# Kernel optimization log

Hardware: AMD Instinct MI355X
Metric: run time of the kernel (lower is better)

Reference implementation:

```python
import jax, jax.numpy as jnp
import numpy as np

EPS = 1e-8  # torch nn.CosineSimilarity default eps


def setup_inputs() -> dict:
    key = jax.random.key(0)
    k1, k2, k3 = jax.random.split(key, 3)
    N, K, Q, CH, H, W, D = 32, 5, 15, 3, 84, 84, 1600
    supp_x = jax.random.normal(k1, (N, K, CH, H, W), dtype=jnp.float32)
    query_x = jax.random.normal(k2, (N, Q, CH, H, W), dtype=jnp.float32)
    W_enc = jax.random.normal(k3, (CH * H * W, D), dtype=jnp.float32) * 0.02
    return {"supp_x": supp_x, "query_x": query_x, "W_enc": W_enc}


def reference(supp_x, query_x, W_enc):
    N, K = supp_x.shape[0], supp_x.shape[1]
    Q = query_x.shape[1]
    # encoder: flatten image -> linear projection (stands in for backbone)
    s_feat = supp_x.reshape(N * K, -1) @ W_enc          # (N*K, D)
    x_proto = s_feat.reshape(N, K, -1).mean(axis=1)     # (N, D) class prototypes
    x_q = query_x.reshape(N * Q, -1) @ W_enc            # (N*Q, D)
    # cosine similarity: L2-normalize with eps clamp, then single matmul
    qn = x_q / jnp.maximum(jnp.linalg.norm(x_q, axis=1, keepdims=True), EPS)
    pn = x_proto / jnp.maximum(jnp.linalg.norm(x_proto, axis=1, keepdims=True), EPS)
    sim = qn @ pn.T                                     # (N*Q, N)
    return jax.nn.log_softmax(sim, axis=1)
```

## Files before the change

kernel.cpp:

```cpp
#include <hip/hip_runtime.h>
#include <cstdint>
#include <cstddef>

namespace {

constexpr int NCLS   = 32;
constexpr int KSHOT  = 5;
constexpr int FDIM   = 21168;
constexpr int KPAD   = 21248;
constexpr int DDIM   = 1600;
constexpr int NROW   = 512;
constexpr int NQROW  = 480;
constexpr int NKT    = 332;
constexpr int MAXS   = 10;

using short8 = __attribute__((ext_vector_type(8))) short;
using f32x4  = __attribute__((ext_vector_type(4))) float;

__device__ __forceinline__ unsigned f2bf(float x) {
    union { float f; unsigned u; } v; v.f = x;
    unsigned r = v.u + 0x7fffu + ((v.u >> 16) & 1u);
    return r >> 16;
}

__global__ void prep_A(const float* __restrict__ supp,
                       const float* __restrict__ query,
                       unsigned short* __restrict__ A) {
    const int r = blockIdx.y;
    const int u = blockIdx.x * blockDim.x + threadIdx.x;
    if (u >= KPAD / 4) return;
    const int c = u * 4;
    float4 v = make_float4(0.f, 0.f, 0.f, 0.f);
    if (c < FDIM) {
        if (r < NCLS) {
            const float* s = supp + (size_t)r * KSHOT * FDIM + c;
            float4 a0 = *(const float4*)(s);
            float4 a1 = *(const float4*)(s + FDIM);
            float4 a2 = *(const float4*)(s + 2 * FDIM);
            float4 a3 = *(const float4*)(s + 3 * FDIM);
            float4 a4 = *(const float4*)(s + 4 * FDIM);
            v.x = (a0.x + a1.x + a2.x + a3.x + a4.x) * 0.2f;
            v.y = (a0.y + a1.y + a2.y + a3.y + a4.y) * 0.2f;
            v.z = (a0.z + a1.z + a2.z + a3.z + a4.z) * 0.2f;
            v.w = (a0.w + a1.w + a2.w + a3.w + a4.w) * 0.2f;
        } else {
            v = *(const float4*)(query + (size_t)(r - NCLS) * FDIM + c);
        }
    }
    ushort4 o;
    o.x = (unsigned short)f2bf(v.x); o.y = (unsigned short)f2bf(v.y);
    o.z = (unsigned short)f2bf(v.z); o.w = (unsigned short)f2bf(v.w);
    *(ushort4*)(A + (size_t)r * KPAD + c) = o;
}

__global__ __launch_bounds__(512, 4) void gemm10(
        const unsigned short* __restrict__ A,
        const float* __restrict__ W,
        float* __restrict__ Cpart, int S) {
    __shared__ unsigned short Al[2][256 * 64];
    __shared__ unsigned short Bl[2][64 * 64];

    const int nwg = gridDim.x, orig = blockIdx.x;
    const int xcd = orig & 7, q8 = nwg >> 3, r8 = nwg & 7;
    const int wgid = (xcd < r8 ? xcd * (q8 + 1) : r8 * (q8 + 1) + (xcd - r8) * q8)
                   + (orig >> 3);

    const int s   = wgid / 50;
    const int rem = wgid % 50;
    const int mt  = rem / 25;
    const int nt  = rem % 25;
    const int m0  = mt * 256;
    const int n0  = nt * 64;
    const int t0  = (NKT * s) / S;
    const int t1  = (NKT * (s + 1)) / S;
    const int tmax = t1 - 1;

    const int tid  = threadIdx.x;
    const int lane = tid & 63;
    const int w    = tid >> 6;
    const int wr   = w & 3;
    const int wc   = w >> 2;
    const int g    = lane >> 4;
    const int r15  = lane & 15;

    const int srow = lane >> 3, sblk = lane & 7;
    const unsigned short* Asrc[4];
    int AdstOff[4];
    #pragma unroll
    for (int i = 0; i < 4; ++i) {
        const int r = w * 32 + i * 8 + srow;
        Asrc[i] = A + (size_t)(m0 + r) * KPAD + (size_t)((sblk ^ (r & 7)) * 8);
        AdstOff[i] = (w * 32 + i * 8) * 64;
    }

    const int np = tid & 31;
    const int kq = tid >> 5;
    const float* Wp = W + n0 + 2 * np;
    const int bws = (kq ^ (2 * (np & 7))) * 4;
    const int wb0 = (2 * np) * 64 + bws;
    const int wb1 = (2 * np + 1) * 64 + bws;

    f32x4 acc[4][2];
    #pragma unroll
    for (int i = 0; i < 4; ++i)
        #pragma unroll
        for (int j = 0; j < 2; ++j)
            acc[i][j] = (f32x4){0.f, 0.f, 0.f, 0.f};

#define SB0() __builtin_amdgcn_sched_barrier(0)

#define GLDS_A(buf, t) { _Pragma("unroll") \
    for (int i = 0; i < 4; ++i) \
        __builtin_amdgcn_global_load_lds( \
            (const __attribute__((address_space(1))) void*)(Asrc[i] + (size_t)(t) * 64), \
            (__attribute__((address_space(3))) void*)(&Al[buf][AdstOff[i]]), 16, 0, 0); }

#define LOAD_W(wv, t) { const int kb_ = (t) * 64 + kq * 4; _Pragma("unroll") \
    for (int i = 0; i < 4; ++i) \
        wv[i] = (kb_ + i < FDIM) ? *(const float2*)(Wp + (size_t)(kb_ + i) * DDIM) \
                                 : make_float2(0.f, 0.f); }

#define PACK_B(buf, wv) { uint2 p0_, p1_; \
    p0_.x = f2bf(wv[0].x) | (f2bf(wv[1].x) << 16); \
    p0_.y = f2bf(wv[2].x) | (f2bf(wv[3].x) << 16); \
    p1_.x = f2bf(wv[0].y) | (f2bf(wv[1].y) << 16); \
    p1_.y = f2bf(wv[2].y) | (f2bf(wv[3].y) << 16); \
    *(uint2*)&Bl[buf][wb0] = p0_; *(uint2*)&Bl[buf][wb1] = p1_; }

#define COMPUTE(buf) { _Pragma("unroll") \
    for (int kk = 0; kk < 2; ++kk) { \
        const int q_ = kk * 4 + g; \
        short8 bf_[2], af_[4]; \
        _Pragma("unroll") \
        for (int ns = 0; ns < 2; ++ns) { \
            const int n_ = wc * 32 + ns * 16 + r15; \
            bf_[ns] = *(const short8*)&Bl[buf][n_ * 64 + ((q_ ^ ((n_ >> 1) & 7)) * 8)]; \
        } \
        _Pragma("unroll") \
        for (int ms = 0; ms < 4; ++ms) { \
            const int R_ = wr * 64 + ms * 16 + r15; \
            af_[ms] = *(const short8*)&Al[buf][R_ * 64 + ((q_ ^ (R_ & 7)) * 8)]; \
        } \
        _Pragma("unroll") \
        for (int ms = 0; ms < 4; ++ms) \
            _Pragma("unroll") \
            for (int ns = 0; ns < 2; ++ns) \
                acc[ms][ns] = __builtin_amdgcn_mfma_f32_16x16x32_bf16( \
                    af_[ms], bf_[ns], acc[ms][ns], 0, 0, 0); } }

    float2 wv0[4], wvA[4], wvB[4];

    LOAD_W(wv0, t0);
    SB0();
    GLDS_A(0, t0);
    SB0();
    PACK_B(0, wv0);
    LOAD_W(wvA, min(t0 + 1, tmax));
    LOAD_W(wvB, min(t0 + 2, tmax));
    asm volatile("s_waitcnt vmcnt(8) lgkmcnt(0)" ::: "memory");
    SB0();
    __builtin_amdgcn_s_barrier();

    int t = t0;
    for (; t + 1 < t1; t += 2) {
        PACK_B(1, wvA);
        GLDS_A(1, t + 1);
        SB0();
        LOAD_W(wvA, min(t + 3, tmax));
        SB0();
        COMPUTE(0);
        asm volatile("s_waitcnt vmcnt(4) lgkmcnt(0)" ::: "memory");
        SB0();
        __builtin_amdgcn_s_barrier();

        PACK_B(0, wvB);
        GLDS_A(0, min(t + 2, tmax));
        SB0();
        LOAD_W(wvB, min(t + 4, tmax));
        SB0();
        COMPUTE(1);
        asm volatile("s_waitcnt vmcnt(4) lgkmcnt(0)" ::: "memory");
        SB0();
        __builtin_amdgcn_s_barrier();
    }
    if (t < t1) {
        COMPUTE(0);
    }

#undef SB0
#undef GLDS_A
#undef LOAD_W
#undef PACK_B
#undef COMPUTE

    float* Cp = Cpart + (size_t)s * NROW * DDIM;
    #pragma unroll
    for (int ms = 0; ms < 4; ++ms) {
        const int row = m0 + wr * 64 + ms * 16 + g * 4;
        #pragma unroll
        for (int ns = 0; ns < 2; ++ns) {
            const int col = n0 + wc * 32 + ns * 16 + r15;
            #pragma unroll
            for (int r = 0; r < 4; ++r)
                Cp[(size_t)(row + r) * DDIM + col] = acc[ms][ns][r];
        }
    }
}

__global__ void reduce_norm(const float* __restrict__ Cpart,
                            float* __restrict__ C,
                            float* __restrict__ inv_norm, int S) {
    const int row = blockIdx.x;
    const int tid = threadIdx.x;
    float acc = 0.f;
    for (int c4 = tid * 4; c4 < DDIM; c4 += 1024) {
        float4 v = make_float4(0.f, 0.f, 0.f, 0.f);
        for (int s2 = 0; s2 < S; ++s2) {
            float4 p = *(const float4*)&Cpart[((size_t)s2 * NROW + row) * DDIM + c4];
            v.x += p.x; v.y += p.y; v.z += p.z; v.w += p.w;
        }
        *(float4*)&C[(size_t)row * DDIM + c4] = v;
        acc += v.x * v.x + v.y * v.y + v.z * v.z + v.w * v.w;
    }
    __shared__ float red[4];
    #pragma unroll
    for (int off = 32; off > 0; off >>= 1) acc += __shfl_xor(acc, off);
    if ((tid & 63) == 0) red[tid >> 6] = acc;
    __syncthreads();
    if (tid == 0) {
        float a = red[0] + red[1] + red[2] + red[3];
        inv_norm[row] = 1.f / fmaxf(sqrtf(a), 1e-8f);
    }
}

__global__ void simlog(const float* __restrict__ C,
                       const float* __restrict__ inv_norm,
                       float* __restrict__ out) {
    __shared__ float qs[DDIM];
    __shared__ float sims[NCLS];
    const int r = blockIdx.x;
    const int tid = threadIdx.x;
    const float* qrow = C + (size_t)(NCLS + r) * DDIM;
    for (int c = tid; c < DDIM; c += 256) qs[c] = qrow[c];
    __syncthreads();
    const float invq = inv_norm[NCLS + r];
    const int lane = tid & 63, w = tid >> 6;
    #pragma unroll
    for (int j = 0; j < 8; ++j) {
        const int p = w * 8 + j;
        const float* prow = C + (size_t)p * DDIM;
        float d = 0.f;
        for (int c = lane; c < DDIM; c += 64) d += qs[c] * prow[c];
        #pragma unroll
        for (int off = 32; off > 0; off >>= 1) d += __shfl_xor(d, off);
        if (lane == 0) sims[p] = d * invq * inv_norm[p];
    }
    __syncthreads();
    if (w == 0) {
        float v = (lane < NCLS) ? sims[lane] : -1e30f;
        float m = v;
        #pragma unroll
        for (int off = 32; off > 0; off >>= 1) m = fmaxf(m, __shfl_xor(m, off));
        float e = (lane < NCLS) ? expf(v - m) : 0.f;
        float ss = e;
        #pragma unroll
        for (int off = 32; off > 0; off >>= 1) ss += __shfl_xor(ss, off);
        if (lane < NCLS) out[(size_t)r * NCLS + lane] = v - m - logf(ss);
    }
}

}


extern "C" void kernel_launch(void* const* d_in, const int* in_sizes, int n_in,
                              void* d_out, int out_size, void* d_ws, size_t ws_size,
                              hipStream_t stream) {
    const float* supp  = (const float*)d_in[0];
    const float* query = (const float*)d_in[1];
    const float* Wenc  = (const float*)d_in[2];
    float* out = (float*)d_out;

    const size_t fixedA = 21757952;
    const size_t slot   = (size_t)NROW * DDIM * 4;

    int S = MAXS;
    if (ws_size > fixedA + slot + 4096) {
        size_t avail = (ws_size - fixedA - slot - 4096) / slot;
        if ((size_t)S > avail) S = (int)avail;
    }
    if (S < 1) S = 1;

    char* ws = (char*)d_ws;
    unsigned short* A = (unsigned short*)ws;
    float* Cpart    = (float*)(ws + fixedA);
    float* C        = (float*)(ws + fixedA + (size_t)S * slot);
    float* inv_norm = (float*)(ws + fixedA + (size_t)(S + 1) * slot);

    hipLaunchKernelGGL(prep_A, dim3((KPAD / 4 + 255) / 256, NROW), dim3(256),
                       0, stream, supp, query, A);
    hipLaunchKernelGGL(gemm10, dim3(50 * S), dim3(512), 0, stream,
                       A, Wenc, Cpart, S);
    hipLaunchKernelGGL(reduce_norm, dim3(NROW), dim3(256), 0, stream,
                       Cpart, C, inv_norm, S);
    hipLaunchKernelGGL(simlog, dim3(NQROW), dim3(256), 0, stream,
                       C, inv_norm, out);
}
```

Baseline: 157.7 us.

## Simplify GEMM pipeline to single-stage prefetch, reorder tiles, extend LDS swizzle

Replaces the hand-scheduled two-deep W register prefetch (explicit waitcnt, sched_barrier, 2x-unrolled loop) with a simpler one-iteration-ahead loop that uses __syncthreads. Tile ordering now interleaves the two M tiles so neighbouring workgroups share the same W column block, which should improve L2 reuse of W. The B LDS swizzle gains an extra XOR term to reduce bank conflicts on writes and reads. The risk is that the shallower prefetch and compiler-inserted waits expose more global load latency.

```diff
diff --git a/kernel.cpp b/kernel.cpp
--- a/kernel.cpp
+++ b/kernel.cpp
@@ -53,7 +53,7 @@
     *(ushort4*)(A + (size_t)r * KPAD + c) = o;
 }
 
-__global__ __launch_bounds__(512, 4) void gemm10(
+__global__ __launch_bounds__(512, 4) void gemm11(
         const unsigned short* __restrict__ A,
         const float* __restrict__ W,
         float* __restrict__ Cpart, int S) {
@@ -67,8 +67,8 @@
 
     const int s   = wgid / 50;
     const int rem = wgid % 50;
-    const int mt  = rem / 25;
-    const int nt  = rem % 25;
+    const int mt  = rem & 1;
+    const int nt  = rem >> 1;
     const int m0  = mt * 256;
     const int n0  = nt * 64;
     const int t0  = (NKT * s) / S;
@@ -96,7 +96,7 @@
     const int np = tid & 31;
     const int kq = tid >> 5;
     const float* Wp = W + n0 + 2 * np;
-    const int bws = (kq ^ (2 * (np & 7))) * 4;
+    const int bws = (kq ^ (2 * (np & 7)) ^ (8 * ((np >> 3) & 1))) * 4;
     const int wb0 = (2 * np) * 64 + bws;
     const int wb1 = (2 * np + 1) * 64 + bws;
 
@@ -107,25 +107,25 @@
         for (int j = 0; j < 2; ++j)
             acc[i][j] = (f32x4){0.f, 0.f, 0.f, 0.f};
 
-#define SB0() __builtin_amdgcn_sched_barrier(0)
+    float2 wv[4];
+
+#define LOAD_W(t) { const int kb_ = (t) * 64 + kq * 4; _Pragma("unroll") \
+    for (int i = 0; i < 4; ++i) \
+        wv[i] = (kb_ + i < FDIM) ? *(const float2*)(Wp + (size_t)(kb_ + i) * DDIM) \
+                                 : make_float2(0.f, 0.f); }
+
+#define PACK_B(buf) { uint2 p0_, p1_; \
+    p0_.x = f2bf(wv[0].x) | (f2bf(wv[1].x) << 16); \
+    p0_.y = f2bf(wv[2].x) | (f2bf(wv[3].x) << 16); \
+    p1_.x = f2bf(wv[0].y) | (f2bf(wv[1].y) << 16); \
+    p1_.y = f2bf(wv[2].y) | (f2bf(wv[3].y) << 16); \
+    *(uint2*)&Bl[buf][wb0] = p0_; *(uint2*)&Bl[buf][wb1] = p1_; }
 
 #define GLDS_A(buf, t) { _Pragma("unroll") \
     for (int i = 0; i < 4; ++i) \
         __builtin_amdgcn_global_load_lds( \
             (const __attribute__((address_space(1))) void*)(Asrc[i] + (size_t)(t) * 64), \
             (__attribute__((address_space(3))) void*)(&Al[buf][AdstOff[i]]), 16, 0, 0); }
-
-#define LOAD_W(wv, t) { const int kb_ = (t) * 64 + kq * 4; _Pragma("unroll") \
-    for (int i = 0; i < 4; ++i) \
-        wv[i] = (kb_ + i < FDIM) ? *(const float2*)(Wp + (size_t)(kb_ + i) * DDIM) \
-                                 : make_float2(0.f, 0.f); }
-
-#define PACK_B(buf, wv) { uint2 p0_, p1_; \
-    p0_.x = f2bf(wv[0].x) | (f2bf(wv[1].x) << 16); \
-    p0_.y = f2bf(wv[2].x) | (f2bf(wv[3].x) << 16); \
-    p1_.x = f2bf(wv[0].y) | (f2bf(wv[1].y) << 16); \
-    p1_.y = f2bf(wv[2].y) | (f2bf(wv[3].y) << 16); \
-    *(uint2*)&Bl[buf][wb0] = p0_; *(uint2*)&Bl[buf][wb1] = p1_; }
 
 #define COMPUTE(buf) { _Pragma("unroll") \
     for (int kk = 0; kk < 2; ++kk) { \
@@ -134,7 +134,8 @@
         _Pragma("unroll") \
         for (int ns = 0; ns < 2; ++ns) { \
             const int n_ = wc * 32 + ns * 16 + r15; \
-            bf_[ns] = *(const short8*)&Bl[buf][n_ * 64 + ((q_ ^ ((n_ >> 1) & 7)) * 8)]; \
+            const int rb_ = q_ ^ ((n_ >> 1) & 7) ^ (4 * ((n_ >> 4) & 1)); \
+            bf_[ns] = *(const short8*)&Bl[buf][n_ * 64 + rb_ * 8]; \
         } \
         _Pragma("unroll") \
         for (int ms = 0; ms < 4; ++ms) { \
@@ -148,49 +149,28 @@
                 acc[ms][ns] = __builtin_amdgcn_mfma_f32_16x16x32_bf16( \
                     af_[ms], bf_[ns], acc[ms][ns], 0, 0, 0); } }
 
-    float2 wv0[4], wvA[4], wvB[4];
-
-    LOAD_W(wv0, t0);
-    SB0();
+    LOAD_W(t0);
+    PACK_B(0);
+    LOAD_W(min(t0 + 1, tmax));
     GLDS_A(0, t0);
-    SB0();
-    PACK_B(0, wv0);
-    LOAD_W(wvA, min(t0 + 1, tmax));
-    LOAD_W(wvB, min(t0 + 2, tmax));
-    asm volatile("s_waitcnt vmcnt(8) lgkmcnt(0)" ::: "memory");
-    SB0();
-    __builtin_amdgcn_s_barrier();
-
-    int t = t0;
-    for (; t + 1 < t1; t += 2) {
-        PACK_B(1, wvA);
-        GLDS_A(1, t + 1);
-        SB0();
-        LOAD_W(wvA, min(t + 3, tmax));
-        SB0();
-        COMPUTE(0);
-        asm volatile("s_waitcnt vmcnt(4) lgkmcnt(0)" ::: "memory");
-        SB0();
-        __builtin_amdgcn_s_barrier();
-
-        PACK_B(0, wvB);
-        GLDS_A(0, min(t + 2, tmax));
-        SB0();
-        LOAD_W(wvB, min(t + 4, tmax));
-        SB0();
-        COMPUTE(1);
-        asm volatile("s_waitcnt vmcnt(4) lgkmcnt(0)" ::: "memory");
-        SB0();
-        __builtin_amdgcn_s_barrier();
-    }
-    if (t < t1) {
-        COMPUTE(0);
-    }
-
-#undef SB0
-#undef GLDS_A
+    __syncthreads();
+
+    int cur = 0;
+    for (int t = t0; t < t1; ++t) {
+        const bool m1 = (t + 1 < t1);
+        if (m1) {
+            PACK_B(cur ^ 1);
+            LOAD_W(min(t + 2, tmax));
+            GLDS_A(cur ^ 1, t + 1);
+        }
+        COMPUTE(cur);
+        __syncthreads();
+        if (m1) cur ^= 1;
+    }
+
 #undef LOAD_W
 #undef PACK_B
+#undef GLDS_A
 #undef COMPUTE
 
     float* Cp = Cpart + (size_t)s * NROW * DDIM;
@@ -298,7 +278,7 @@
 
     hipLaunchKernelGGL(prep_A, dim3((KPAD / 4 + 255) / 256, NROW), dim3(256),
                        0, stream, supp, query, A);
-    hipLaunchKernelGGL(gemm10, dim3(50 * S), dim3(512), 0, stream,
+    hipLaunchKernelGGL(gemm11, dim3(50 * S), dim3(512), 0, stream,
                        A, Wenc, Cpart, S);
     hipLaunchKernelGGL(reduce_norm, dim3(NROW), dim3(256), 0, stream,
                        Cpart, C, inv_norm, S);
```

Measured after the change: 132.2 us. -16.2%, faster.
